# Kernel optimization log

Hardware: AMD Instinct MI355X
Metric: run time of the kernel (lower is better)

The kernel has to match this reference:

```python
import jax, jax.numpy as jnp
import numpy as np

N, E, B, IN = 20000, 320000, 64, 192


def setup_inputs() -> dict:
    key = jax.random.key(0)
    ks = iter(jax.random.split(key, 80))
    d = {}
    d["x"] = jax.random.normal(next(ks), (N, IN), jnp.float32)
    d["edge_index"] = jax.random.randint(next(ks), (2, E), 0, N - 1)  # +1 shift stays < N
    d["edge_attr"] = jax.random.normal(next(ks), (E,), jnp.float32)
    d["batch"] = jnp.sort(jax.random.randint(next(ks), (N,), 0, B))

    def lin(i, o):
        w = jax.random.normal(next(ks), (i, o), jnp.float32) * (1.0 / i ** 0.5)
        return w, jnp.zeros((o,), jnp.float32)

    dims = [(IN, 4, 64), (256, 4, 64), (256, 6, 32)]  # (in_ch, heads, out_ch) per conv
    for l, (ic, h, c) in enumerate(dims, 1):
        hc = h * c
        d[f"Wq{l}"], d[f"bq{l}"] = lin(ic, hc)
        d[f"Wk{l}"], d[f"bk{l}"] = lin(ic, hc)
        d[f"Wv{l}"], d[f"bv{l}"] = lin(ic, hc)
        d[f"We{l}"] = jax.random.normal(next(ks), (1, hc), jnp.float32)  # lin_edge, no bias
        d[f"Ws{l}"], d[f"bs{l}"] = lin(ic, hc)  # root/skip weight
    d["g1"] = jnp.ones((256,), jnp.float32); d["be1"] = jnp.zeros((256,), jnp.float32)
    d["g2"] = jnp.ones((256,), jnp.float32); d["be2"] = jnp.zeros((256,), jnp.float32)
    d["fc1_w"], d["fc1_b"] = lin(192, 32)
    d["fc2_w"], d["fc2_b"] = lin(32, 2)
    return d


def seg_softmax(s, seg, n):
    # per-destination-node softmax over edges, [E, H]
    m = jax.ops.segment_max(s, seg, num_segments=n)
    m = jnp.where(jnp.isfinite(m), m, 0.0)
    ex = jnp.exp(s - m[seg])
    den = jax.ops.segment_sum(ex, seg, num_segments=n)
    return ex / (den[seg] + 1e-16)


def tconv(x, src, dst, e, Wq, bq, Wk, bk, Wv, bv, We, Ws, bs, h, c):
    # PyG TransformerConv (concat=True, root_weight=True, beta=False, eval -> no dropout)
    n = x.shape[0]
    q = (x @ Wq + bq).reshape(n, h, c)
    k = (x @ Wk + bk).reshape(n, h, c)
    v = (x @ Wv + bv).reshape(n, h, c)
    ee = (e @ We).reshape(-1, h, c)           # [E, h, c] edge embedding
    kj = k[src] + ee                           # gather keys along edges
    scores = jnp.einsum('ehc,ehc->eh', q[dst], kj) * (1.0 / c ** 0.5)
    alpha = seg_softmax(scores, dst, n)        # [E, h]
    msg = (v[src] + ee) * alpha[..., None]
    out = jax.ops.segment_sum(msg, dst, num_segments=n).reshape(n, h * c)
    return out + x @ Ws + bs, alpha


def ln(x, g, b):
    mu = x.mean(-1, keepdims=True)
    var = x.var(-1, keepdims=True)
    return g * (x - mu) / jnp.sqrt(var + 1e-5) + b


def _forward(x, edge_index, edge_attr, batch, Wq1, bq1, Wk1, bk1, Wv1, bv1, We1, Ws1, bs1, Wq2, bq2, Wk2, bk2, Wv2, bv2, We2, Ws2, bs2, Wq3, bq3, Wk3, bk3, Wv3, bv3, We3, Ws3, bs3, g1, be1, g2, be2, fc1_w, fc1_b, fc2_w, fc2_b):
    ei = edge_index + 1                       # replicates `edge_index += 1` in source
    src, dst = ei[0], ei[1]
    e = edge_attr[:, None]                    # edge_dim = 1
    x1, a1 = tconv(x, src, dst, e, Wq1, bq1, Wk1, bk1, Wv1, bv1, We1, Ws1, bs1, 4, 64)
    x1 = jax.nn.relu(ln(x1, g1, be1))
    x2, a2 = tconv(x1, src, dst, e, Wq2, bq2, Wk2, bk2, Wv2, bv2, We2, Ws2, bs2, 4, 64)
    x2 = jax.nn.relu(ln(x2, g2, be2))
    x3, a3 = tconv(x2, src, dst, e, Wq3, bq3, Wk3, bk3, Wv3, bv3, We3, Ws3, bs3, 6, 32)
    x3 = jax.nn.relu(x3)                      # note: norm3 exists in __init__ but is never applied
    xr = x + x3
    cnt = jax.ops.segment_sum(jnp.ones((xr.shape[0],), xr.dtype), batch, num_segments=B)
    pooled = jax.ops.segment_sum(xr, batch, num_segments=B) / jnp.maximum(cnt, 1.0)[:, None]
    h = jax.nn.relu(pooled @ fc1_w + fc1_b)
    logits = h @ fc2_w + fc2_b
    return logits, a1, a2, a3


def reference(x, edge_index, edge_attr, batch, Wq1, bq1, Wk1, bk1, Wv1, bv1, We1, Ws1, bs1, Wq2, bq2, Wk2, bk2, Wv2, bv2, We2, Ws2, bs2, Wq3, bq3, Wk3, bk3, Wv3, bv3, We3, Ws3, bs3, g1, be1, g2, be2, fc1_w, fc1_b, fc2_w, fc2_b):
    return _forward(x, edge_index, edge_attr, batch, Wq1, bq1, Wk1, bk1, Wv1, bv1, We1, Ws1, bs1, Wq2, bq2, Wk2, bk2, Wv2, bv2, We2, Ws2, bs2, Wq3, bq3, Wk3, bk3, Wv3, bv3, We3, Ws3, bs3, g1, be1, g2, be2, fc1_w, fc1_b, fc2_w, fc2_b)
```

## Files before the change

### kernel.cpp

```cpp
#include <hip/hip_runtime.h>
#include <cstdint>
#include <cstddef>

#define DEVINL __device__ __forceinline__

typedef short s16x8 __attribute__((ext_vector_type(8)));
typedef float f32x4 __attribute__((ext_vector_type(4)));
typedef unsigned short u16x4 __attribute__((ext_vector_type(4)));
typedef unsigned short u16x8 __attribute__((ext_vector_type(8)));

DEVINL unsigned short f2bf(float f) {
  unsigned u = __float_as_uint(f);
  unsigned r = (u + 0x7FFFu + ((u >> 16) & 1u)) >> 16;
  return (unsigned short)r;
}
DEVINL float bf2f(unsigned short b) { return __uint_as_float(((unsigned)b) << 16); }

__global__ __launch_bounds__(256) void fill_i32(int* __restrict__ p, int val, int n) {
  int i = blockIdx.x * 256 + threadIdx.x;
  if (i < n) p[i] = val;
}


__global__ __launch_bounds__(256) void cvt_split(const float* __restrict__ in,
                                                 unsigned short* __restrict__ hi,
                                                 unsigned short* __restrict__ lo, int n) {
  int i = blockIdx.x * 256 + threadIdx.x;
  if (i >= n) return;
  float f = in[i];
  unsigned short h = f2bf(f);
  float r = f - bf2f(h);
  hi[i] = h;
  lo[i] = f2bf(r);
}

struct CvtWArgs {
  const float* W[12];
  int K[12];
  int M[12];
};
__global__ __launch_bounds__(256) void cvt_w_all(CvtWArgs a,
                                                 unsigned short* __restrict__ Wh,
                                                 unsigned short* __restrict__ Wl) {
  int tid = blockIdx.x * 256 + threadIdx.x;
  int mat = tid >> 16;
  int off = tid & 65535;
  if (mat >= 12) return;
  int K = a.K[mat], M = a.M[mat];
  if (off >= K * M) return;
  int k = off / M, m = off - k * M;
  float f = a.W[mat][off];
  unsigned short h = f2bf(f);
  float r = f - bf2f(h);
  size_t dst = (size_t)mat * 65536 + (size_t)m * K + k;
  Wh[dst] = h;
  Wl[dst] = f2bf(r);
}

struct GemmArgs {
  const unsigned short* Wh[4];
  const unsigned short* Wl[4];
  const float* bias[4];
  float* out[4];
  int obf[4];
};

template <int KTOT>
__global__ __launch_bounds__(256, 3) void gemm4_lds(
    const unsigned short* __restrict__ Ah, const unsigned short* __restrict__ Al,
    GemmArgs args, int N, int M) {
  const int BK = 64;
  __shared__ unsigned short ash[128 * 64];
  __shared__ unsigned short asl[128 * 64];
  __shared__ unsigned short wsh[64 * 64];
  __shared__ unsigned short wsl[64 * 64];
  int tid = threadIdx.x;
  int wave = tid >> 6, lane = tid & 63;
  int lrow = lane & 15, quad = lane >> 4;
  int mt = M >> 6;
  int ntile = mt * 4;
  int id = blockIdx.x, nwg = gridDim.x;
  int q8 = nwg >> 3, r8 = nwg & 7;
  int xcd = id & 7, j8 = id >> 3;
  int wg = (xcd < r8 ? xcd * (q8 + 1) : r8 * (q8 + 1) + (xcd - r8) * q8) + j8;
  int by = wg / ntile;
  int bxx = wg - by * ntile;
  int z = bxx / mt;
  int colTile = bxx - z * mt;
  int row0 = by * 128;
  int col0 = colTile * 64;
  const unsigned short* __restrict__ Wh = args.Wh[z];
  const unsigned short* __restrict__ Wl = args.Wl[z];
  const bool full = (args.obf[z] == 0);

  int ar[4], asq[4];
  size_t agoff[4];
#pragma unroll
  for (int i = 0; i < 4; i++) {
    int c = tid + i * 256;
    ar[i] = c >> 3;
    int kq = c & 7;
    asq[i] = kq ^ (ar[i] & 7);
    int gr = row0 + ar[i]; if (gr >= N) gr = N - 1;
    agoff[i] = (size_t)gr * KTOT + kq * 8;
  }
  int wr[2], wsq[2];
  size_t wgoff[2];
#pragma unroll
  for (int i = 0; i < 2; i++) {
    int c = tid + i * 256;
    wr[i] = c >> 3;
    int kq = c & 7;
    wsq[i] = kq ^ (wr[i] & 7);
    wgoff[i] = (size_t)(col0 + wr[i]) * KTOT + kq * 8;
  }

  s16x8 pa_h[4], pa_l[4], pw_h[2], pw_l[2];
#pragma unroll
  for (int i = 0; i < 4; i++) {
    pa_h[i] = *(const s16x8*)(Ah + agoff[i]);
    pa_l[i] = *(const s16x8*)(Al + agoff[i]);
  }
#pragma unroll
  for (int i = 0; i < 2; i++) {
    pw_h[i] = *(const s16x8*)(Wh + wgoff[i]);
    if (full) pw_l[i] = *(const s16x8*)(Wl + wgoff[i]);
  }

  f32x4 acc[2][4] = {};

  for (int k0 = 0; k0 < KTOT; k0 += BK) {
    __syncthreads();
#pragma unroll
    for (int i = 0; i < 4; i++) {
      *(s16x8*)(ash + ar[i] * 64 + asq[i] * 8) = pa_h[i];
      *(s16x8*)(asl + ar[i] * 64 + asq[i] * 8) = pa_l[i];
    }
#pragma unroll
    for (int i = 0; i < 2; i++) {
      *(s16x8*)(wsh + wr[i] * 64 + wsq[i] * 8) = pw_h[i];
      if (full) *(s16x8*)(wsl + wr[i] * 64 + wsq[i] * 8) = pw_l[i];
    }
    if (k0 + BK < KTOT) {
      int kn = k0 + BK;
#pragma unroll
      for (int i = 0; i < 4; i++) {
        pa_h[i] = *(const s16x8*)(Ah + agoff[i] + kn);
        pa_l[i] = *(const s16x8*)(Al + agoff[i] + kn);
      }
#pragma unroll
      for (int i = 0; i < 2; i++) {
        pw_h[i] = *(const s16x8*)(Wh + wgoff[i] + kn);
        if (full) pw_l[i] = *(const s16x8*)(Wl + wgoff[i] + kn);
      }
    }
    __syncthreads();
#pragma unroll
    for (int kk = 0; kk < 2; kk++) {
      s16x8 fah[2], fal[2], fbh[4], fbl[4];
#pragma unroll
      for (int rf = 0; rf < 2; rf++) {
        int r = wave * 32 + rf * 16 + lrow;
        int sq = (kk * 4 + quad) ^ (lrow & 7);
        fah[rf] = *(const s16x8*)(ash + r * 64 + sq * 8);
        fal[rf] = *(const s16x8*)(asl + r * 64 + sq * 8);
      }
#pragma unroll
      for (int cf = 0; cf < 4; cf++) {
        int cc = cf * 16 + lrow;
        int sq = (kk * 4 + quad) ^ (lrow & 7);
        fbh[cf] = *(const s16x8*)(wsh + cc * 64 + sq * 8);
        if (full) fbl[cf] = *(const s16x8*)(wsl + cc * 64 + sq * 8);
      }
#pragma unroll
      for (int rf = 0; rf < 2; rf++)
#pragma unroll
        for (int cf = 0; cf < 4; cf++) {
          acc[rf][cf] = __builtin_amdgcn_mfma_f32_16x16x32_bf16(fah[rf], fbh[cf], acc[rf][cf], 0, 0, 0);
          acc[rf][cf] = __builtin_amdgcn_mfma_f32_16x16x32_bf16(fal[rf], fbh[cf], acc[rf][cf], 0, 0, 0);
          if (full)
            acc[rf][cf] = __builtin_amdgcn_mfma_f32_16x16x32_bf16(fah[rf], fbl[cf], acc[rf][cf], 0, 0, 0);
        }
    }
  }
  const float* __restrict__ bias = args.bias[z];
  int obf = args.obf[z];
  if (obf == 0) {
    float* __restrict__ C = args.out[z];
#pragma unroll
    for (int cf = 0; cf < 4; cf++) {
      int col = col0 + cf * 16 + lrow;
      float bv = bias[col];
#pragma unroll
      for (int rf = 0; rf < 2; rf++) {
        int rb = row0 + wave * 32 + rf * 16 + quad * 4;
#pragma unroll
        for (int r = 0; r < 4; r++) {
          int rr = rb + r;
          if (rr < N) C[(size_t)rr * M + col] = acc[rf][cf][r] + bv;
        }
      }
    }
  } else {
    __syncthreads();
#pragma unroll
    for (int cf = 0; cf < 4; cf++) {
      int col = cf * 16 + lrow;
      float bv = bias[col0 + col];
#pragma unroll
      for (int rf = 0; rf < 2; rf++) {
        int rl = wave * 32 + rf * 16 + quad * 4;
#pragma unroll
        for (int r = 0; r < 4; r++)
          ash[(rl + r) * 64 + col] = f2bf(acc[rf][cf][r] + bv);
      }
    }
    __syncthreads();
    unsigned short* __restrict__ C = (unsigned short*)args.out[z];
#pragma unroll
    for (int i = 0; i < 4; i++) {
      int c = tid + i * 256;
      int row = c >> 3, g8 = c & 7;
      int rr = row0 + row;
      if (rr < N)
        *(u16x8*)(C + (size_t)rr * M + col0 + g8 * 8) =
            *(const u16x8*)(ash + row * 64 + g8 * 8);
    }
  }
}


__global__ __launch_bounds__(256) void hist_dst(const int* __restrict__ dst,
                                                int* __restrict__ cnt, int E) {
  int e = blockIdx.x * 256 + threadIdx.x;
  if (e < E) atomicAdd(&cnt[dst[e] + 1], 1);
}

__global__ __launch_bounds__(1024) void scan_hist(const int* __restrict__ cnt,
                                                  int* __restrict__ start,
                                                  int* __restrict__ off, int N) {
  __shared__ int sums[1024];
  const int CH = 20;
  int t = threadIdx.x;
  int base = t * CH;
  int local[CH];
  int tot = 0;
  if (base < N) {
#pragma unroll
    for (int i = 0; i < CH; i++) { local[i] = cnt[base + i]; tot += local[i]; }
  }
  sums[t] = tot;
  __syncthreads();
  for (int d = 1; d < 1024; d <<= 1) {
    int v = (t >= d) ? sums[t - d] : 0;
    __syncthreads();
    sums[t] += v;
    __syncthreads();
  }
  if (base < N) {
    int run = (t == 0) ? 0 : sums[t - 1];
#pragma unroll
    for (int i = 0; i < CH; i++) { start[base + i] = run; off[base + i] = run; run += local[i]; }
    if (base + CH == N) start[N] = run;
  }
}

__global__ __launch_bounds__(256) void scatter_edges(
    const int* __restrict__ src, const int* __restrict__ dst,
    const float* __restrict__ ea, int* __restrict__ off,
    int* __restrict__ src_s, float* __restrict__ ea_s, int* __restrict__ eid_s, int E) {
  int e = blockIdx.x * 256 + threadIdx.x;
  if (e >= E) return;
  int d = dst[e] + 1;
  int pos = atomicAdd(&off[d], 1);
  src_s[pos] = src[e] + 1;
  ea_s[pos] = ea[e];
  eid_s[pos] = e;
}

template <int H, int LPH>
__global__ __launch_bounds__(256) void attn_fused(
    const unsigned short* __restrict__ q, const unsigned short* __restrict__ kb,
    const unsigned short* __restrict__ vb, const float* __restrict__ We,
    const int* __restrict__ start, const int* __restrict__ src_s,
    const float* __restrict__ ea_s, const int* __restrict__ eid_s,
    float* __restrict__ sc, float* __restrict__ outp,
    float* __restrict__ alpha, int Nn, float scale) {
  const int HC = H * LPH * 4;
  int w = (blockIdx.x * 256 + threadIdx.x) >> 6;
  int lane = threadIdx.x & 63;
  if (w >= Nn) return;
  int b = start[w], e = start[w + 1];
  if (b == e) return;
  bool act = lane < H * LPH;
  int idx = lane * 4;
  int head = lane / LPH;
  float4 q4 = make_float4(0.f, 0.f, 0.f, 0.f), We4 = q4;
  if (act) {
    u16x4 qv = *(const u16x4*)(q + (size_t)w * HC + idx);
    q4.x = bf2f(qv.x); q4.y = bf2f(qv.y); q4.z = bf2f(qv.z); q4.w = bf2f(qv.w);
    We4 = *(const float4*)(We + idx);
  }
  float qwe = q4.x * We4.x + q4.y * We4.y + q4.z * We4.z + q4.w * We4.w;
#pragma unroll
  for (int mm = 1; mm < LPH; mm <<= 1) qwe += __shfl_xor(qwe, mm, 64);

  float l = 0.f, tv = 0.f;
  float4 accv = make_float4(0.f, 0.f, 0.f, 0.f);

  auto step = [&](u16x4 kc, u16x4 vc, float eav, int pos) {
    float p = q4.x * bf2f(kc.x) + q4.y * bf2f(kc.y) +
              q4.z * bf2f(kc.z) + q4.w * bf2f(kc.w);
#pragma unroll
    for (int mm = 1; mm < LPH; mm <<= 1) p += __shfl_xor(p, mm, 64);
    float es = __expf((p + eav * qwe) * scale);
    if (act && (lane % LPH) == 0) sc[(size_t)pos * H + head] = es;
    l += es;
    tv = fmaf(es, eav, tv);
    accv.x = fmaf(es, bf2f(vc.x), accv.x);
    accv.y = fmaf(es, bf2f(vc.y), accv.y);
    accv.z = fmaf(es, bf2f(vc.z), accv.z);
    accv.w = fmaf(es, bf2f(vc.w), accv.w);
  };

  u16x4 z4 = {0, 0, 0, 0};
  u16x4 kS[4] = {z4, z4, z4, z4};
  u16x4 vS[4] = {z4, z4, z4, z4};
  float eaS[4] = {0.f, 0.f, 0.f, 0.f};

  auto preload = [&](int pos, int st) {
    int s = src_s[pos]; eaS[st] = ea_s[pos];
    if (act) {
      kS[st] = *(const u16x4*)(kb + (size_t)s * HC + idx);
      vS[st] = *(const u16x4*)(vb + (size_t)s * HC + idx);
    }
  };

#pragma unroll
  for (int j = 0; j < 4; j++) if (b + j < e) preload(b + j, j);

  for (int pos = b; pos < e; pos += 4) {
#pragma unroll
    for (int j = 0; j < 4; j++) {
      if (pos + j < e) {
        u16x4 kc = kS[j];
        u16x4 vc = vS[j];
        float ec = eaS[j];
        if (pos + j + 4 < e) preload(pos + j + 4, j);
        step(kc, vc, ec, pos + j);
      }
    }
  }

  float invl = 1.0f / (l + 1e-16f);
  if (act) {
    float* orow = outp + (size_t)w * HC + idx;
    float4 o = *(float4*)orow;
    o.x += (accv.x + tv * We4.x) * invl;
    o.y += (accv.y + tv * We4.y) * invl;
    o.z += (accv.z + tv * We4.z) * invl;
    o.w += (accv.w + tv * We4.w) * invl;
    *(float4*)orow = o;
  }
  {
    int len = e - b;
    const int PCH = 64 / H;
    int p_of = lane / H;
    int h_of = lane - p_of * H;
    float myinv = __shfl(invl, h_of * LPH, 64);
    __threadfence_block();
    for (int base = 0; base < len; base += PCH) {
      int po = base + p_of;
      if (p_of < PCH && po < len) {
        int pos = b + po;
        float es = sc[(size_t)pos * H + h_of];
        alpha[(size_t)eid_s[pos] * H + h_of] = es * myinv;
      }
    }
  }
}


__global__ __launch_bounds__(256) void ln_relu_split(
    const float* __restrict__ in, const float* __restrict__ g,
    const float* __restrict__ b, unsigned short* __restrict__ hi,
    unsigned short* __restrict__ lo, int N) {
  int w = (blockIdx.x * 256 + threadIdx.x) >> 6;
  int lane = threadIdx.x & 63;
  if (w >= N) return;
  float4 x = *(const float4*)(in + (size_t)w * 256 + lane * 4);
  float s = x.x + x.y + x.z + x.w;
  float s2 = x.x * x.x + x.y * x.y + x.z * x.z + x.w * x.w;
  for (int m = 1; m < 64; m <<= 1) { s += __shfl_xor(s, m, 64); s2 += __shfl_xor(s2, m, 64); }
  float mu = s * (1.0f / 256.0f);
  float var = s2 * (1.0f / 256.0f) - mu * mu;
  float inv = rsqrtf(var + 1e-5f);
  float4 gv = *(const float4*)(g + lane * 4);
  float4 bv = *(const float4*)(b + lane * 4);
  float4 y;
  y.x = fmaxf(fmaf((x.x - mu) * inv, gv.x, bv.x), 0.f);
  y.y = fmaxf(fmaf((x.y - mu) * inv, gv.y, bv.y), 0.f);
  y.z = fmaxf(fmaf((x.z - mu) * inv, gv.z, bv.z), 0.f);
  y.w = fmaxf(fmaf((x.w - mu) * inv, gv.w, bv.w), 0.f);
  u16x4 yh, yl;
  yh.x = f2bf(y.x); yl.x = f2bf(y.x - bf2f(yh.x));
  yh.y = f2bf(y.y); yl.y = f2bf(y.y - bf2f(yh.y));
  yh.z = f2bf(y.z); yl.z = f2bf(y.z - bf2f(yh.z));
  yh.w = f2bf(y.w); yl.w = f2bf(y.w - bf2f(yh.w));
  *(u16x4*)(hi + (size_t)w * 256 + lane * 4) = yh;
  *(u16x4*)(lo + (size_t)w * 256 + lane * 4) = yl;
}

__global__ __launch_bounds__(192) void resid_pool2(
    const float* __restrict__ x, const float* __restrict__ x3,
    const int* __restrict__ batch, float* __restrict__ pooled,
    float* __restrict__ cnt, int N, int R) {
  int col = threadIdx.x;
  int r0 = blockIdx.x * R;
  int r1 = min(r0 + R, N);
  if (r0 >= N) return;
  float acc = 0.f;
  int cur = batch[r0];
  int run = 0;
  for (int r = r0; r < r1; r++) {
    int b = batch[r];
    if (b != cur) {
      atomicAdd(&pooled[cur * 192 + col], acc);
      if (col == 0) atomicAdd(&cnt[cur], (float)run);
      acc = 0.f; run = 0; cur = b;
    }
    size_t i = (size_t)r * 192 + col;
    acc += x[i] + fmaxf(x3[i], 0.f);
    run++;
  }
  atomicAdd(&pooled[cur * 192 + col], acc);
  if (col == 0) atomicAdd(&cnt[cur], (float)run);
}

__global__ __launch_bounds__(64) void head_mlp(
    const float* __restrict__ pooled, const float* __restrict__ cnt,
    const float* __restrict__ fc1w, const float* __restrict__ fc1b,
    const float* __restrict__ fc2w, const float* __restrict__ fc2b,
    float* __restrict__ logits) {
  int b = blockIdx.x;
  int t = threadIdx.x;
  __shared__ float p[192];
  __shared__ float hbuf[32];
  float inv = 1.0f / fmaxf(cnt[b], 1.0f);
  for (int i = t; i < 192; i += 64) p[i] = pooled[b * 192 + i] * inv;
  __syncthreads();
  if (t < 32) {
    float acc = fc1b[t];
    for (int i = 0; i < 192; i++) acc = fmaf(p[i], fc1w[i * 32 + t], acc);
    hbuf[t] = fmaxf(acc, 0.f);
  }
  __syncthreads();
  if (t < 2) {
    float acc = fc2b[t];
    for (int j = 0; j < 32; j++) acc = fmaf(hbuf[j], fc2w[j * 2 + t], acc);
    logits[b * 2 + t] = acc;
  }
}

static inline int divup(int a, int b) { return (a + b - 1) / b; }

extern "C" void kernel_launch(void* const* d_in, const int* in_sizes, int n_in,
                              void* d_out, int out_size, void* d_ws, size_t ws_size,
                              hipStream_t stream) {
  const int N = 20000, E = 320000, B = 64;
  const float* x     = (const float*)d_in[0];
  const int*   ei    = (const int*)d_in[1];
  const float* eattr = (const float*)d_in[2];
  const int*   batch = (const int*)d_in[3];
  const int* srcp = ei;
  const int* dstp = ei + E;

  const float* Wq[3]; const float* bq[3]; const float* Wk[3]; const float* bk[3];
  const float* Wv[3]; const float* bv[3]; const float* We[3]; const float* Ws[3];
  const float* bs[3];
  for (int l = 0; l < 3; l++) {
    int base = 4 + l * 9;
    Wq[l] = (const float*)d_in[base + 0]; bq[l] = (const float*)d_in[base + 1];
    Wk[l] = (const float*)d_in[base + 2]; bk[l] = (const float*)d_in[base + 3];
    Wv[l] = (const float*)d_in[base + 4]; bv[l] = (const float*)d_in[base + 5];
    We[l] = (const float*)d_in[base + 6];
    Ws[l] = (const float*)d_in[base + 7]; bs[l] = (const float*)d_in[base + 8];
  }
  const float* g1  = (const float*)d_in[31]; const float* be1 = (const float*)d_in[32];
  const float* g2  = (const float*)d_in[33]; const float* be2 = (const float*)d_in[34];
  const float* fc1w = (const float*)d_in[35]; const float* fc1b = (const float*)d_in[36];
  const float* fc2w = (const float*)d_in[37]; const float* fc2b = (const float*)d_in[38];

  float* out = (float*)d_out;
  float* logits = out;
  float* a1 = out + 128;
  float* a2 = a1 + (size_t)E * 4;
  float* a3 = a2 + (size_t)E * 4;

  float* ws = (float*)d_ws;
  size_t o = 0;
  float* qb = ws + o; o += (size_t)N * 256;
  float* kvb = ws + o; o += (size_t)N * 256;
  float* xa = ws + o; o += (size_t)N * 256;
  float* xb = ws + o; o += (size_t)N * 256;
  float* sc = ws + o; o += (size_t)E * 6;
  int*   cntb  = (int*)(ws + o); o += N;
  int*   startb= (int*)(ws + o); o += N + 1;
  int*   offb  = (int*)(ws + o); o += N + 1;
  int*   src_s = (int*)(ws + o); o += E;
  float* ea_s  = ws + o; o += E;
  int*   eid_s = (int*)(ws + o); o += E;
  float* pooled = ws + o; o += (size_t)B * 192;
  float* cnt    = ws + o; o += B;
  unsigned short* Ah = (unsigned short*)(ws + o); o += (size_t)N * 128;
  unsigned short* Al = (unsigned short*)(ws + o); o += (size_t)N * 128;
  unsigned short* Wh12 = (unsigned short*)(ws + o); o += (size_t)12 * 32768;
  unsigned short* Wl12 = (unsigned short*)(ws + o); o += (size_t)12 * 32768;

  unsigned short* qh = (unsigned short*)qb;
  unsigned short* kh = (unsigned short*)kvb;
  unsigned short* vh = kh + (size_t)N * 256;

  dim3 blk(256);

  struct LayerCfg { int K, M; float scale; };
  LayerCfg cfg[3] = {
    {192, 256, 0.125f},
    {256, 256, 0.125f},
    {256, 192, 0.1767766952966369f},
  };
  CvtWArgs cwa;
  for (int l = 0; l < 3; l++) {
    cwa.W[l * 4 + 0] = Wq[l]; cwa.W[l * 4 + 1] = Wk[l];
    cwa.W[l * 4 + 2] = Wv[l]; cwa.W[l * 4 + 3] = Ws[l];
    for (int zz = 0; zz < 4; zz++) {
      cwa.K[l * 4 + zz] = cfg[l].K; cwa.M[l * 4 + zz] = cfg[l].M;
    }
  }
  cvt_w_all<<<12 * 65536 / 256, blk, 0, stream>>>(cwa, Wh12, Wl12);

  fill_i32<<<divup(N, 256), blk, 0, stream>>>(cntb, 0, N);
  hist_dst<<<divup(E, 256), blk, 0, stream>>>(dstp, cntb, E);
  scan_hist<<<1, dim3(1024), 0, stream>>>(cntb, startb, offb, N);
  scatter_edges<<<divup(E, 256), blk, 0, stream>>>(srcp, dstp, eattr, offb,
                                                  src_s, ea_s, eid_s, E);

  float*       lay_out[3] = {xa, xb, xa};
  float*       alpha_out[3] = {a1, a2, a3};

  cvt_split<<<divup(N * 192, 256), blk, 0, stream>>>(x, Ah, Al, N * 192);

  int stripes = divup(N, 128);
  for (int l = 0; l < 3; l++) {
    int M = cfg[l].M;
    GemmArgs ga;
    float* outs[4] = {(float*)qh, (float*)kh, (float*)vh, lay_out[l]};
    const float* biases[4] = {bq[l], bk[l], bv[l], bs[l]};
    int obfs[4] = {1, 1, 1, 0};
    for (int z = 0; z < 4; z++) {
      ga.Wh[z] = Wh12 + (size_t)(l * 4 + z) * 65536;
      ga.Wl[z] = Wl12 + (size_t)(l * 4 + z) * 65536;
      ga.bias[z] = biases[z];
      ga.out[z] = outs[z];
      ga.obf[z] = obfs[z];
    }
    dim3 gg((M >> 6) * 4 * stripes);
    if (l == 0)      gemm4_lds<192><<<gg, blk, 0, stream>>>(Ah, Al, ga, N, M);
    else             gemm4_lds<256><<<gg, blk, 0, stream>>>(Ah, Al, ga, N, M);

    dim3 gat(divup(N * 64, 256));
    if (l < 2) {
      attn_fused<4, 16><<<gat, blk, 0, stream>>>(qh, kh, vh, We[l], startb, src_s,
                                                 ea_s, eid_s, sc, lay_out[l],
                                                 alpha_out[l], N, cfg[l].scale);
    } else {
      attn_fused<6, 8><<<gat, blk, 0, stream>>>(qh, kh, vh, We[l], startb, src_s,
                                                ea_s, eid_s, sc, lay_out[l],
                                                alpha_out[l], N, cfg[l].scale);
    }
    if (l == 0) ln_relu_split<<<divup(N, 4), blk, 0, stream>>>(xa, g1, be1, Ah, Al, N);
    if (l == 1) ln_relu_split<<<divup(N, 4), blk, 0, stream>>>(xb, g2, be2, Ah, Al, N);
  }

  fill_i32<<<divup(B * 192 + B, 256), blk, 0, stream>>>((int*)pooled, 0, B * 192 + B);
  resid_pool2<<<divup(N, 32), dim3(192), 0, stream>>>(x, xa, batch, pooled, cnt, N, 32);
  head_mlp<<<B, dim3(64), 0, stream>>>(pooled, cnt, fc1w, fc1b, fc2w, fc2b, logits);
}
```

Before: 589.5 us.

## Process two edges per wavefront in attention with 8-wide bf16 lanes

```diff
diff --git a/kernel.cpp b/kernel.cpp
--- a/kernel.cpp
+++ b/kernel.cpp
@@ -278,7 +278,7 @@
   eid_s[pos] = e;
 }
 
-template <int H, int LPH>
+template <int H, int ACT>
 __global__ __launch_bounds__(256) void attn_fused(
     const unsigned short* __restrict__ q, const unsigned short* __restrict__ kb,
     const unsigned short* __restrict__ vb, const float* __restrict__ We,
@@ -286,88 +286,115 @@
     const float* __restrict__ ea_s, const int* __restrict__ eid_s,
     float* __restrict__ sc, float* __restrict__ outp,
     float* __restrict__ alpha, int Nn, float scale) {
-  const int HC = H * LPH * 4;
+  const int HC = ACT * 8;
+  const int LPH2 = ACT / H;
   int w = (blockIdx.x * 256 + threadIdx.x) >> 6;
   int lane = threadIdx.x & 63;
   if (w >= Nn) return;
   int b = start[w], e = start[w + 1];
   if (b == e) return;
-  bool act = lane < H * LPH;
-  int idx = lane * 4;
-  int head = lane / LPH;
-  float4 q4 = make_float4(0.f, 0.f, 0.f, 0.f), We4 = q4;
+  int hlane = lane & 31, half = lane >> 5;
+  bool act = hlane < ACT;
+  int idx = hlane * 8;
+  int head = hlane / LPH2;
+  float q8[8], We8[8];
+#pragma unroll
+  for (int j = 0; j < 8; j++) { q8[j] = 0.f; We8[j] = 0.f; }
   if (act) {
-    u16x4 qv = *(const u16x4*)(q + (size_t)w * HC + idx);
-    q4.x = bf2f(qv.x); q4.y = bf2f(qv.y); q4.z = bf2f(qv.z); q4.w = bf2f(qv.w);
-    We4 = *(const float4*)(We + idx);
-  }
-  float qwe = q4.x * We4.x + q4.y * We4.y + q4.z * We4.z + q4.w * We4.w;
-#pragma unroll
-  for (int mm = 1; mm < LPH; mm <<= 1) qwe += __shfl_xor(qwe, mm, 64);
+    u16x8 qv = *(const u16x8*)(q + (size_t)w * HC + idx);
+#pragma unroll
+    for (int j = 0; j < 8; j++) q8[j] = bf2f(qv[j]);
+    float4 w0 = *(const float4*)(We + idx);
+    float4 w1 = *(const float4*)(We + idx + 4);
+    We8[0] = w0.x; We8[1] = w0.y; We8[2] = w0.z; We8[3] = w0.w;
+    We8[4] = w1.x; We8[5] = w1.y; We8[6] = w1.z; We8[7] = w1.w;
+  }
+  float qwe = 0.f;
+#pragma unroll
+  for (int j = 0; j < 8; j++) qwe = fmaf(q8[j], We8[j], qwe);
+#pragma unroll
+  for (int mm = 1; mm < LPH2; mm <<= 1) qwe += __shfl_xor(qwe, mm, 64);
 
   float l = 0.f, tv = 0.f;
-  float4 accv = make_float4(0.f, 0.f, 0.f, 0.f);
-
-  auto step = [&](u16x4 kc, u16x4 vc, float eav, int pos) {
-    float p = q4.x * bf2f(kc.x) + q4.y * bf2f(kc.y) +
-              q4.z * bf2f(kc.z) + q4.w * bf2f(kc.w);
-#pragma unroll
-    for (int mm = 1; mm < LPH; mm <<= 1) p += __shfl_xor(p, mm, 64);
+  float accv[8] = {0.f, 0.f, 0.f, 0.f, 0.f, 0.f, 0.f, 0.f};
+
+  auto step = [&](u16x8 kc, u16x8 vc, float eav, int pairpos) {
+    bool vld = (pairpos + half) < e;
+    float p = 0.f;
+#pragma unroll
+    for (int j = 0; j < 8; j++) p = fmaf(q8[j], bf2f(kc[j]), p);
+#pragma unroll
+    for (int mm = 1; mm < LPH2; mm <<= 1) p += __shfl_xor(p, mm, 64);
     float es = __expf((p + eav * qwe) * scale);
-    if (act && (lane % LPH) == 0) sc[(size_t)pos * H + head] = es;
+    if (!vld) es = 0.f;
+    if (act && vld && (hlane % LPH2) == 0)
+      sc[(size_t)(pairpos + half) * H + head] = es;
     l += es;
     tv = fmaf(es, eav, tv);
-    accv.x = fmaf(es, bf2f(vc.x), accv.x);
-    accv.y = fmaf(es, bf2f(vc.y), accv.y);
-    accv.z = fmaf(es, bf2f(vc.z), accv.z);
-    accv.w = fmaf(es, bf2f(vc.w), accv.w);
+#pragma unroll
+    for (int j = 0; j < 8; j++) accv[j] = fmaf(es, bf2f(vc[j]), accv[j]);
   };
 
-  u16x4 z4 = {0, 0, 0, 0};
-  u16x4 kS[4] = {z4, z4, z4, z4};
-  u16x4 vS[4] = {z4, z4, z4, z4};
+  u16x8 z8 = {0, 0, 0, 0, 0, 0, 0, 0};
+  u16x8 kS[4] = {z8, z8, z8, z8};
+  u16x8 vS[4] = {z8, z8, z8, z8};
   float eaS[4] = {0.f, 0.f, 0.f, 0.f};
 
-  auto preload = [&](int pos, int st) {
-    int s = src_s[pos]; eaS[st] = ea_s[pos];
+  auto preload = [&](int pairpos, int st) {
+    int pp = pairpos + half;
+    int pc = pp < e ? pp : (e - 1);
+    int s = src_s[pc];
+    eaS[st] = ea_s[pc];
     if (act) {
-      kS[st] = *(const u16x4*)(kb + (size_t)s * HC + idx);
-      vS[st] = *(const u16x4*)(vb + (size_t)s * HC + idx);
+      kS[st] = *(const u16x8*)(kb + (size_t)s * HC + idx);
+      vS[st] = *(const u16x8*)(vb + (size_t)s * HC + idx);
     }
   };
 
 #pragma unroll
-  for (int j = 0; j < 4; j++) if (b + j < e) preload(b + j, j);
-
-  for (int pos = b; pos < e; pos += 4) {
+  for (int j = 0; j < 4; j++) if (b + 2 * j < e) preload(b + 2 * j, j);
+
+  for (int pos = b; pos < e; pos += 8) {
 #pragma unroll
     for (int j = 0; j < 4; j++) {
-      if (pos + j < e) {
-        u16x4 kc = kS[j];
-        u16x4 vc = vS[j];
+      int pp = pos + 2 * j;
+      if (pp < e) {
+        u16x8 kc = kS[j];
+        u16x8 vc = vS[j];
         float ec = eaS[j];
-        if (pos + j + 4 < e) preload(pos + j + 4, j);
-        step(kc, vc, ec, pos + j);
-      }
-    }
-  }
+        if (pp + 8 < e) preload(pp + 8, j);
+        step(kc, vc, ec, pp);
+      }
+    }
+  }
+
+  l += __shfl_xor(l, 32, 64);
+  tv += __shfl_xor(tv, 32, 64);
+#pragma unroll
+  for (int j = 0; j < 8; j++) accv[j] += __shfl_xor(accv[j], 32, 64);
 
   float invl = 1.0f / (l + 1e-16f);
-  if (act) {
+  if (act && half == 0) {
     float* orow = outp + (size_t)w * HC + idx;
-    float4 o = *(float4*)orow;
-    o.x += (accv.x + tv * We4.x) * invl;
-    o.y += (accv.y + tv * We4.y) * invl;
-    o.z += (accv.z + tv * We4.z) * invl;
-    o.w += (accv.w + tv * We4.w) * invl;
-    *(float4*)orow = o;
+    float4 o0 = *(float4*)orow;
+    float4 o1 = *(float4*)(orow + 4);
+    o0.x += (accv[0] + tv * We8[0]) * invl;
+    o0.y += (accv[1] + tv * We8[1]) * invl;
+    o0.z += (accv[2] + tv * We8[2]) * invl;
+    o0.w += (accv[3] + tv * We8[3]) * invl;
+    o1.x += (accv[4] + tv * We8[4]) * invl;
+    o1.y += (accv[5] + tv * We8[5]) * invl;
+    o1.z += (accv[6] + tv * We8[6]) * invl;
+    o1.w += (accv[7] + tv * We8[7]) * invl;
+    *(float4*)orow = o0;
+    *(float4*)(orow + 4) = o1;
   }
   {
     int len = e - b;
     const int PCH = 64 / H;
     int p_of = lane / H;
     int h_of = lane - p_of * H;
-    float myinv = __shfl(invl, h_of * LPH, 64);
+    float myinv = __shfl(invl, h_of * LPH2, 64);
     __threadfence_block();
     for (int base = 0; base < len; base += PCH) {
       int po = base + p_of;
@@ -570,13 +597,13 @@
 
     dim3 gat(divup(N * 64, 256));
     if (l < 2) {
-      attn_fused<4, 16><<<gat, blk, 0, stream>>>(qh, kh, vh, We[l], startb, src_s,
+      attn_fused<4, 32><<<gat, blk, 0, stream>>>(qh, kh, vh, We[l], startb, src_s,
                                                  ea_s, eid_s, sc, lay_out[l],
                                                  alpha_out[l], N, cfg[l].scale);
     } else {
-      attn_fused<6, 8><<<gat, blk, 0, stream>>>(qh, kh, vh, We[l], startb, src_s,
-                                                ea_s, eid_s, sc, lay_out[l],
-                                                alpha_out[l], N, cfg[l].scale);
+      attn_fused<6, 24><<<gat, blk, 0, stream>>>(qh, kh, vh, We[l], startb, src_s,
+                                                 ea_s, eid_s, sc, lay_out[l],
+                                                 alpha_out[l], N, cfg[l].scale);
     }
     if (l == 0) ln_relu_split<<<divup(N, 4), blk, 0, stream>>>(xa, g1, be1, Ah, Al, N);
     if (l == 1) ln_relu_split<<<divup(N, 4), blk, 0, stream>>>(xb, g2, be2, Ah, Al, N);
```

Result: no change. 584.1 us (-0.9%).
